# Optimization experiments

Measured on AMD Instinct MI355X. Metric: run time of the kernel, lower is better.

The kernel has to match this reference:

```python
import jax, jax.numpy as jnp
import numpy as np

N_EMBD = 256


def setup_inputs() -> dict:
    key = jax.random.key(0)
    kx, kq, kk, kv = jax.random.split(key, 4)
    B, S, D = 4, 4096, N_EMBD
    scale = 1.0 / np.sqrt(D)
    x = jax.random.normal(kx, (B, S, D), dtype=jnp.float32)
    # nn.Linear(D, D, bias=False) weights; torch applies x @ W.T
    Wq = jax.random.normal(kq, (D, D), dtype=jnp.float32) * scale
    Wk = jax.random.normal(kk, (D, D), dtype=jnp.float32) * scale
    Wv = jax.random.normal(kv, (D, D), dtype=jnp.float32) * scale
    return {"x": x, "Wq": Wq, "Wk": Wk, "Wv": Wv}


def reference(x, Wq, Wk, Wv):
    B, S, D = x.shape
    q = jnp.einsum('bsd,ed->bse', x, Wq)
    k = jnp.einsum('bsd,ed->bse', x, Wk)
    v = jnp.einsum('bsd,ed->bse', x, Wv)
    scale = 1.0 / jnp.sqrt(jnp.asarray(D, dtype=x.dtype))
    scores = jnp.einsum('bqd,bkd->bqk', q, k) * scale  # [B,S,S]
    causal = jnp.tril(jnp.ones((S, S), dtype=bool))
    masked = jnp.where(causal[None, :, :], scores, jnp.asarray(-jnp.inf, dtype=scores.dtype))
    weights = jax.nn.softmax(masked, axis=-1)
    out = jnp.einsum('bqk,bkd->bqd', weights, v)
    return out
```

## Files before the change

### kernel.cpp

```cpp
#include <hip/hip_runtime.h>
#include <hip/hip_bf16.h>


#define SEQ 4096
#define DIM 256
#define NBATCH 4
#define KVBLK 64
#define KVT_BYTES 65536

#define QB_OFF   0
#define KV_OFF   (8u*1024*1024)
#define O1_OFF   (24u*1024*1024)
#define O2_OFF   (32u*1024*1024)
#define O3_OFF   (40u*1024*1024)
#define ML_OFF   (48u*1024*1024)

#define QSCALE 0.09016844f
#define DEFER_THR 11.5415603f

typedef __attribute__((ext_vector_type(8))) short bf16x8;
typedef __attribute__((ext_vector_type(4))) float f32x4;
typedef __attribute__((ext_vector_type(4))) unsigned short us4;

static __device__ inline unsigned short f2bf(float f) {
  unsigned int u = __float_as_uint(f);
  u += 0x7FFFu + ((u >> 16) & 1u);
  return (unsigned short)(u >> 16);
}
static __device__ inline float bf2f(unsigned short u) {
  return __uint_as_float(((unsigned int)u) << 16);
}

__global__ __launch_bounds__(256) void qkv_gemm(
    const float* __restrict__ x, const float* __restrict__ Wq,
    const float* __restrict__ Wk, const float* __restrict__ Wv,
    char* __restrict__ qbf, char* __restrict__ kv)
{
  __shared__ unsigned short A_lds[128][40];
  __shared__ unsigned short B_lds[3][64][40];

  const int tid = threadIdx.x;
  const int lane = tid & 63;
  const int w = tid >> 6;
  const int lo = lane & 15, hi = lane >> 4;
  const int mb = blockIdx.x * 128;
  const int nb = blockIdx.y * 64;
  const float* Ws[3] = { Wq, Wk, Wv };

  f32x4 acc[3][2][4];
#pragma unroll
  for (int z = 0; z < 3; z++)
#pragma unroll
    for (int mi = 0; mi < 2; mi++)
#pragma unroll
      for (int ni = 0; ni < 4; ni++) acc[z][mi][ni] = (f32x4){0.f, 0.f, 0.f, 0.f};

  for (int ks = 0; ks < 8; ++ks) {
    const int k0 = ks * 32;
    __syncthreads();
#pragma unroll
    for (int i = 0; i < 4; ++i) {
      int f = tid + i * 256;
      int row = f >> 3, c4 = (f & 7) * 4;
      float4 v = *(const float4*)(x + (size_t)(mb + row) * DIM + k0 + c4);
      us4 bv = { f2bf(v.x), f2bf(v.y), f2bf(v.z), f2bf(v.w) };
      *(us4*)&A_lds[row][c4] = bv;
    }
#pragma unroll
    for (int z = 0; z < 3; z++)
#pragma unroll
      for (int i = 0; i < 2; ++i) {
        int f = tid + i * 256;
        int row = f >> 3, c4 = (f & 7) * 4;
        float4 v = *(const float4*)(Ws[z] + (size_t)(nb + row) * DIM + k0 + c4);
        us4 bv = { f2bf(v.x), f2bf(v.y), f2bf(v.z), f2bf(v.w) };
        *(us4*)&B_lds[z][row][c4] = bv;
      }
    __syncthreads();
    bf16x8 a[2];
#pragma unroll
    for (int mi = 0; mi < 2; mi++) a[mi] = *(const bf16x8*)&A_lds[w * 32 + mi * 16 + lo][hi * 8];
#pragma unroll
    for (int z = 0; z < 3; z++) {
      bf16x8 bfr[4];
#pragma unroll
      for (int ni = 0; ni < 4; ni++) bfr[ni] = *(const bf16x8*)&B_lds[z][ni * 16 + lo][hi * 8];
#pragma unroll
      for (int mi = 0; mi < 2; mi++)
#pragma unroll
        for (int ni = 0; ni < 4; ni++)
          acc[z][mi][ni] = __builtin_amdgcn_mfma_f32_16x16x32_bf16(a[mi], bfr[ni], acc[z][mi][ni], 0, 0, 0);
    }
  }

#pragma unroll
  for (int mi = 0; mi < 2; mi++) {
    int r0 = mb + w * 32 + mi * 16 + hi * 4;
#pragma unroll
    for (int ni = 0; ni < 4; ni++) {
      int d = nb + ni * 16 + lo;
      int kkq = d >> 5, hiq = (d >> 3) & 3, eq = d & 7;
#pragma unroll
      for (int j = 0; j < 4; j++) {
        int srow = r0 + j;
        int s16 = srow >> 4, loq = srow & 15;
        size_t byte = ((size_t)(s16 * 8 + kkq) << 10) + ((hiq * 16 + loq) << 4) + eq * 2;
        *(unsigned short*)(qbf + byte) = f2bf(acc[0][mi][ni][j] * QSCALE);
      }
    }
  }
#pragma unroll
  for (int mi = 0; mi < 2; mi++) {
    int r0 = mb + w * 32 + mi * 16 + hi * 4;
#pragma unroll
    for (int ni = 0; ni < 4; ni++) {
      int d = nb + ni * 16 + lo;
      int kkk = d >> 5, hik = (d >> 3) & 3, ek = d & 7;
#pragma unroll
      for (int j = 0; j < 4; j++) {
        int srow = r0 + j;
        int bb = srow >> 12, sl = srow & 4095;
        int t = sl >> 6, r = sl & 63;
        int nf = r >> 4, lok = r & 15;
        size_t byte = ((size_t)(bb * 64 + t)) * KVT_BYTES +
                      ((size_t)(nf * 8 + kkk) << 10) + ((hik * 16 + lok) << 4) + ek * 2;
        *(unsigned short*)(kv + byte) = f2bf(acc[1][mi][ni][j]);
      }
    }
  }
#pragma unroll
  for (int mi = 0; mi < 2; mi++) {
    int s0 = mb + w * 32 + mi * 16 + hi * 4;
    int bb = s0 >> 12;
    int t = (s0 >> 6) & 63;
    int s_t = s0 & 63;
    int ksI = s_t >> 5;
    int hf = (s_t >> 3) & 3;
    int e0 = s_t & 7;
#pragma unroll
    for (int ni = 0; ni < 4; ni++) {
      int d = nb + ni * 16 + lo;
      int n = d >> 4;
      us4 pv = { f2bf(acc[2][mi][ni][0]), f2bf(acc[2][mi][ni][1]),
                 f2bf(acc[2][mi][ni][2]), f2bf(acc[2][mi][ni][3]) };
      size_t byte = ((size_t)(bb * 64 + t)) * KVT_BYTES + 32768 +
                    ((size_t)(ksI * 16 + n) << 10) + ((hf * 16 + lo) << 4) + e0 * 2;
      *(us4*)(kv + byte) = pv;
    }
  }
}

__global__ __launch_bounds__(512, 1) void attn_fa(
    const char* __restrict__ qbf, const char* __restrict__ kv,
    float* __restrict__ out, unsigned short* __restrict__ o1,
    unsigned short* __restrict__ o2, unsigned short* __restrict__ o3,
    float* __restrict__ ml)
{
  __shared__ char KV_lds[2][KVT_BYTES];
  __shared__ unsigned short P_lds[8][16][72];

  const int tid = threadIdx.x;
  const int lane = tid & 63;
  const int w = tid >> 6;
  const int lo = lane & 15, hi = lane >> 4;
  const int id = blockIdx.x;
  const int x = id & 7;
  const int b = x >> 1;
  const int v = id >> 3;
  const int p = v & 15;
  const int cbase = ((v >> 4) << 1) | (x & 1);

  const char* kv_base = kv + (size_t)b * 64 * KVT_BYTES;

  auto stageKV = [&](int t, int buf) {
    const char* src = kv_base + (size_t)t * KVT_BYTES + tid * 16;
    char* dst = &KV_lds[buf][0] + tid * 16;
#pragma unroll
    for (int i = 0; i < 8; ++i) {
      __builtin_amdgcn_global_load_lds(
          (const __attribute__((address_space(1))) void*)(src + i * 8192),
          (__attribute__((address_space(3))) void*)(dst + i * 8192),
          16, 0, 0);
    }
  };

  for (int task = 0; task < 2; ++task) {
    const int u = task ? (15 - p) + 16 : p;
    const int cc = task ? (3 - cbase) : cbase;
    const int nt = 2 * u + 2;
    const int t0 = (nt * cc) >> 2;
    const int t1 = (nt * (cc + 1)) >> 2;
    const int qrow0 = u * 128 + w * 16;
    const int rbase = b * SEQ + qrow0;
    float* mlc = ml + (size_t)cc * 16384 * 2;

    if (t0 >= t1) {
      if (lane < 16) {
        mlc[(size_t)(rbase + lane) * 2 + 0] = -3e38f;
        mlc[(size_t)(rbase + lane) * 2 + 1] = 0.f;
      }
      if (cc == 0) {
#pragma unroll
        for (int j = 0; j < 16; j++)
#pragma unroll
          for (int n = 0; n < 4; n++)
            out[(size_t)(rbase + j) * DIM + n * 64 + lane] = 0.f;
      }
      continue;
    }

    bf16x8 qf[8];
    {
      const char* qp = qbf + ((size_t)(b * 256 + u * 8 + w) << 13) + lane * 16;
#pragma unroll
      for (int kk = 0; kk < 8; kk++)
        qf[kk] = *(const bf16x8*)(qp + kk * 1024);
    }

    stageKV(t0, 0);
    if (t0 + 1 < t1) stageKV(t0 + 1, 1);

    float m_run[4], l_run[4];
#pragma unroll
    for (int j = 0; j < 4; j++) { m_run[j] = -3e38f; l_run[j] = 0.f; }
    f32x4 o_acc[16];
#pragma unroll
    for (int n = 0; n < 16; n++) o_acc[n] = (f32x4){0.f, 0.f, 0.f, 0.f};

    for (int t = t0; t < t1; ++t) {
      const int cur = (t - t0) & 1;

      if (t + 1 < t1) {
        asm volatile("s_waitcnt vmcnt(8)" ::: "memory");
      } else {
        asm volatile("s_waitcnt vmcnt(0)" ::: "memory");
      }
      __builtin_amdgcn_sched_barrier(0);
      __builtin_amdgcn_s_barrier();

      const char* kt = &KV_lds[cur][0] + lane * 16;

      f32x4 sf[4];
      __builtin_amdgcn_s_setprio(1);
#pragma unroll
      for (int nf = 0; nf < 4; nf++) {
        bf16x8 kf[8];
#pragma unroll
        for (int kk = 0; kk < 8; kk++)
          kf[kk] = *(const bf16x8*)(kt + ((nf * 8 + kk) << 10));
        f32x4 a = (f32x4){0.f, 0.f, 0.f, 0.f};
#pragma unroll
        for (int kk = 0; kk < 8; kk++)
          a = __builtin_amdgcn_mfma_f32_16x16x32_bf16(qf[kk], kf[kk], a, 0, 0, 0);
        sf[nf] = a;
      }
      __builtin_amdgcn_s_setprio(0);

      const char* vt = &KV_lds[cur][32768] + lane * 16;
      bf16x8 va[16];
#pragma unroll
      for (int i = 0; i < 16; i++)
        va[i] = *(const bf16x8*)(vt + (i << 10));

      if ((t * KVBLK + KVBLK - 1) > qrow0) {
#pragma unroll
        for (int nf = 0; nf < 4; nf++) {
          int kg = t * KVBLK + nf * 16 + lo;
#pragma unroll
          for (int j = 0; j < 4; j++) {
            int qg = qrow0 + hi * 4 + j;
            if (kg > qg) sf[nf][j] = -__builtin_inff();
          }
        }
      }

      float vnew[4];
#pragma unroll
      for (int j = 0; j < 4; j++) {
        float m = fmaxf(fmaxf(sf[0][j], sf[1][j]), fmaxf(sf[2][j], sf[3][j]));
        m = fmaxf(m, __shfl_xor(m, 1));
        m = fmaxf(m, __shfl_xor(m, 2));
        m = fmaxf(m, __shfl_xor(m, 4));
        m = fmaxf(m, __shfl_xor(m, 8));
        vnew[j] = m;
      }
      bool grow = false;
#pragma unroll
      for (int j = 0; j < 4; j++) grow = grow || (vnew[j] > m_run[j] + DEFER_THR);
      if (__any(grow)) {
#pragma unroll
        for (int j = 0; j < 4; j++) {
          float mn = fmaxf(m_run[j], vnew[j]);
          float alpha = exp2f(m_run[j] - mn);
          m_run[j] = mn;
          l_run[j] *= alpha;
#pragma unroll
          for (int n = 0; n < 16; n++) o_acc[n][j] *= alpha;
        }
      }
#pragma unroll
      for (int j = 0; j < 4; j++) {
        float sum = 0.f;
#pragma unroll
        for (int nf = 0; nf < 4; nf++) {
          sf[nf][j] = exp2f(sf[nf][j] - m_run[j]);
          sum += sf[nf][j];
        }
        l_run[j] += sum;
      }

#pragma unroll
      for (int nf = 0; nf < 4; nf++)
#pragma unroll
        for (int j = 0; j < 4; j++)
          P_lds[w][hi * 4 + j][nf * 16 + lo] = f2bf(sf[nf][j]);
      asm volatile("s_waitcnt lgkmcnt(0)" ::: "memory");
      __builtin_amdgcn_sched_barrier(0);
      bf16x8 pa0 = *(const bf16x8*)&P_lds[w][lo][hi * 8];
      bf16x8 pa1 = *(const bf16x8*)&P_lds[w][lo][32 + hi * 8];
      asm volatile("s_waitcnt lgkmcnt(0)" ::: "memory");
      __builtin_amdgcn_sched_barrier(0);

      __builtin_amdgcn_s_setprio(1);
#pragma unroll
      for (int g = 0; g < 4; g++) {
        bf16x8 vb[4];
#pragma unroll
        for (int k = 0; k < 4; k++)
          vb[k] = *(const bf16x8*)(vt + ((16 + g * 4 + k) << 10));
#pragma unroll
        for (int k = 0; k < 4; k++) {
          int n = g * 4 + k;
          o_acc[n] = __builtin_amdgcn_mfma_f32_16x16x32_bf16(pa0, va[n], o_acc[n], 0, 0, 0);
          o_acc[n] = __builtin_amdgcn_mfma_f32_16x16x32_bf16(pa1, vb[k], o_acc[n], 0, 0, 0);
        }
      }
      __builtin_amdgcn_s_setprio(0);

      __builtin_amdgcn_sched_barrier(0);
      __builtin_amdgcn_s_barrier();
      if (t + 2 < t1) stageKV(t + 2, cur);
    }

    unsigned short* opc = (cc == 1) ? o1 : (cc == 2) ? o2 : o3;
#pragma unroll
    for (int j = 0; j < 4; j++) {
      float lsum = l_run[j];
      lsum += __shfl_xor(lsum, 1);
      lsum += __shfl_xor(lsum, 2);
      lsum += __shfl_xor(lsum, 4);
      lsum += __shfl_xor(lsum, 8);
      int r = rbase + hi * 4 + j;
      float inv = (lsum > 0.f) ? 1.f / lsum : 0.f;
      if (cc == 0) {
        float* orow = out + (size_t)r * DIM;
#pragma unroll
        for (int n = 0; n < 16; n++)
          orow[n * 16 + lo] = o_acc[n][j] * inv;
      } else {
        unsigned short* orow = opc + (size_t)r * DIM;
#pragma unroll
        for (int n = 0; n < 16; n++)
          orow[n * 16 + lo] = f2bf(o_acc[n][j] * inv);
      }
      if (lo == 0) {
        mlc[(size_t)r * 2 + 0] = m_run[j];
        mlc[(size_t)r * 2 + 1] = lsum;
      }
    }
  }
}

__global__ __launch_bounds__(256) void merge4(
    const float* __restrict__ ml,
    const unsigned short* __restrict__ o1, const unsigned short* __restrict__ o2,
    const unsigned short* __restrict__ o3, float* __restrict__ out)
{
  int r = blockIdx.x * 4 + (threadIdx.x >> 6);
  int c4 = (threadIdx.x & 63) * 4;
  float m0 = ml[(size_t)r*2],           l0 = ml[(size_t)r*2+1];
  float m1 = ml[(size_t)(16384+r)*2],   l1 = ml[(size_t)(16384+r)*2+1];
  float m2 = ml[(size_t)(32768+r)*2],   l2 = ml[(size_t)(32768+r)*2+1];
  float m3 = ml[(size_t)(49152+r)*2],   l3 = ml[(size_t)(49152+r)*2+1];
  float M = fmaxf(fmaxf(m0, m1), fmaxf(m2, m3));
  float w0 = l0 * exp2f(m0 - M);
  float w1 = l1 * exp2f(m1 - M);
  float w2 = l2 * exp2f(m2 - M);
  float w3 = l3 * exp2f(m3 - M);
  float inv = 1.f / (w0 + w1 + w2 + w3);
  float4 o0 = *(const float4*)(out + (size_t)r * DIM + c4);
  us4 a  = *(const us4*)(o1 + (size_t)r * DIM + c4);
  us4 bq = *(const us4*)(o2 + (size_t)r * DIM + c4);
  us4 cq = *(const us4*)(o3 + (size_t)r * DIM + c4);
  float4 res;
  res.x = (w0*o0.x + w1*bf2f(a.x) + w2*bf2f(bq.x) + w3*bf2f(cq.x)) * inv;
  res.y = (w0*o0.y + w1*bf2f(a.y) + w2*bf2f(bq.y) + w3*bf2f(cq.y)) * inv;
  res.z = (w0*o0.z + w1*bf2f(a.z) + w2*bf2f(bq.z) + w3*bf2f(cq.z)) * inv;
  res.w = (w0*o0.w + w1*bf2f(a.w) + w2*bf2f(bq.w) + w3*bf2f(cq.w)) * inv;
  *(float4*)(out + (size_t)r * DIM + c4) = res;
}

extern "C" void kernel_launch(void* const* d_in, const int* in_sizes, int n_in,
                              void* d_out, int out_size, void* d_ws, size_t ws_size,
                              hipStream_t stream) {
  const float* x  = (const float*)d_in[0];
  const float* Wq = (const float*)d_in[1];
  const float* Wk = (const float*)d_in[2];
  const float* Wv = (const float*)d_in[3];
  char* ws = (char*)d_ws;
  char* qbf = ws + QB_OFF;
  char* kv  = ws + KV_OFF;
  unsigned short* o1 = (unsigned short*)(ws + O1_OFF);
  unsigned short* o2 = (unsigned short*)(ws + O2_OFF);
  unsigned short* o3 = (unsigned short*)(ws + O3_OFF);
  float* ml = (float*)(ws + ML_OFF);
  float* out = (float*)d_out;

  qkv_gemm<<<dim3(128, 4), 256, 0, stream>>>(x, Wq, Wk, Wv, qbf, kv);
  attn_fa<<<dim3(256), 512, 0, stream>>>(qbf, kv, out, o1, o2, o3, ml);
  merge4<<<dim3(4096), 256, 0, stream>>>(ml, o1, o2, o3, out);
}
```

Measured before the change: 96.08 us.

## Compute transposed QK^T scores so each lane owns one query row

Swaps the MFMA operands so the score tile is K·Q^T, giving each lane a single query row with 16 key values. The per-row max and sum reductions then take two cross-lane shuffles instead of four per row, and the running max and sum become scalars per lane. P is packed into LDS with v_cvt_pk_bf16_f32 as 32-bit writes instead of 16 scalar bf16 stores. In exchange, rescaling the output accumulator and the final normalization now need per-row shuffles to fetch alpha and inv.

Measured after the change: 87.21 us. -9.2%, faster.

```diff
diff --git a/kernel.cpp b/kernel.cpp
--- a/kernel.cpp
+++ b/kernel.cpp
@@ -220,9 +220,7 @@
     stageKV(t0, 0);
     if (t0 + 1 < t1) stageKV(t0 + 1, 1);
 
-    float m_run[4], l_run[4];
-#pragma unroll
-    for (int j = 0; j < 4; j++) { m_run[j] = -3e38f; l_run[j] = 0.f; }
+    float m_run = -3e38f, l_run = 0.f;
     f32x4 o_acc[16];
 #pragma unroll
     for (int n = 0; n < 16; n++) o_acc[n] = (f32x4){0.f, 0.f, 0.f, 0.f};
@@ -240,7 +238,7 @@
 
       const char* kt = &KV_lds[cur][0] + lane * 16;
 
-      f32x4 sf[4];
+      f32x4 sfT[4];
       __builtin_amdgcn_s_setprio(1);
 #pragma unroll
       for (int nf = 0; nf < 4; nf++) {
@@ -251,8 +249,8 @@
         f32x4 a = (f32x4){0.f, 0.f, 0.f, 0.f};
 #pragma unroll
         for (int kk = 0; kk < 8; kk++)
-          a = __builtin_amdgcn_mfma_f32_16x16x32_bf16(qf[kk], kf[kk], a, 0, 0, 0);
-        sf[nf] = a;
+          a = __builtin_amdgcn_mfma_f32_16x16x32_bf16(kf[kk], qf[kk], a, 0, 0, 0);
+        sfT[nf] = a;
       }
       __builtin_amdgcn_s_setprio(0);
 
@@ -263,57 +261,59 @@
         va[i] = *(const bf16x8*)(vt + (i << 10));
 
       if ((t * KVBLK + KVBLK - 1) > qrow0) {
+        int qg = qrow0 + lo;
 #pragma unroll
         for (int nf = 0; nf < 4; nf++) {
-          int kg = t * KVBLK + nf * 16 + lo;
 #pragma unroll
           for (int j = 0; j < 4; j++) {
-            int qg = qrow0 + hi * 4 + j;
-            if (kg > qg) sf[nf][j] = -__builtin_inff();
+            int kg = t * KVBLK + nf * 16 + hi * 4 + j;
+            if (kg > qg) sfT[nf][j] = -__builtin_inff();
           }
         }
       }
 
-      float vnew[4];
-#pragma unroll
-      for (int j = 0; j < 4; j++) {
-        float m = fmaxf(fmaxf(sf[0][j], sf[1][j]), fmaxf(sf[2][j], sf[3][j]));
-        m = fmaxf(m, __shfl_xor(m, 1));
-        m = fmaxf(m, __shfl_xor(m, 2));
-        m = fmaxf(m, __shfl_xor(m, 4));
-        m = fmaxf(m, __shfl_xor(m, 8));
-        vnew[j] = m;
-      }
-      bool grow = false;
-#pragma unroll
-      for (int j = 0; j < 4; j++) grow = grow || (vnew[j] > m_run[j] + DEFER_THR);
-      if (__any(grow)) {
+      float vnew = sfT[0][0];
+#pragma unroll
+      for (int nf = 0; nf < 4; nf++)
+#pragma unroll
+        for (int j = 0; j < 4; j++) vnew = fmaxf(vnew, sfT[nf][j]);
+      vnew = fmaxf(vnew, __shfl_xor(vnew, 16));
+      vnew = fmaxf(vnew, __shfl_xor(vnew, 32));
+
+      if (__any(vnew > m_run + DEFER_THR)) {
+        float mn = fmaxf(m_run, vnew);
+        float alpha = exp2f(m_run - mn);
+        m_run = mn;
+        l_run *= alpha;
 #pragma unroll
         for (int j = 0; j < 4; j++) {
-          float mn = fmaxf(m_run[j], vnew[j]);
-          float alpha = exp2f(m_run[j] - mn);
-          m_run[j] = mn;
-          l_run[j] *= alpha;
-#pragma unroll
-          for (int n = 0; n < 16; n++) o_acc[n][j] *= alpha;
+          float aj = __shfl(alpha, (lane & 48) + ((lane >> 4) & 3) * 4 + j);
+#pragma unroll
+          for (int n = 0; n < 16; n++) o_acc[n][j] *= aj;
         }
       }
-#pragma unroll
-      for (int j = 0; j < 4; j++) {
+      {
         float sum = 0.f;
 #pragma unroll
-        for (int nf = 0; nf < 4; nf++) {
-          sf[nf][j] = exp2f(sf[nf][j] - m_run[j]);
-          sum += sf[nf][j];
+        for (int nf = 0; nf < 4; nf++)
+#pragma unroll
+          for (int j = 0; j < 4; j++) {
+            sfT[nf][j] = exp2f(sfT[nf][j] - m_run);
+            sum += sfT[nf][j];
+          }
+        l_run += sum;
+      }
+
+#pragma unroll
+      for (int nf = 0; nf < 4; nf++) {
+#pragma unroll
+        for (int h2 = 0; h2 < 2; h2++) {
+          unsigned int pk;
+          asm("v_cvt_pk_bf16_f32 %0, %1, %2"
+              : "=v"(pk) : "v"(sfT[nf][h2 * 2]), "v"(sfT[nf][h2 * 2 + 1]));
+          *(unsigned int*)&P_lds[w][lo][nf * 16 + hi * 4 + h2 * 2] = pk;
         }
-        l_run[j] += sum;
-      }
-
-#pragma unroll
-      for (int nf = 0; nf < 4; nf++)
-#pragma unroll
-        for (int j = 0; j < 4; j++)
-          P_lds[w][hi * 4 + j][nf * 16 + lo] = f2bf(sf[nf][j]);
+      }
       asm volatile("s_waitcnt lgkmcnt(0)" ::: "memory");
       __builtin_amdgcn_sched_barrier(0);
       bf16x8 pa0 = *(const bf16x8*)&P_lds[w][lo][hi * 8];
@@ -342,31 +342,30 @@
       if (t + 2 < t1) stageKV(t + 2, cur);
     }
 
+    l_run += __shfl_xor(l_run, 16);
+    l_run += __shfl_xor(l_run, 32);
+    float inv = (l_run > 0.f) ? 1.f / l_run : 0.f;
+
     unsigned short* opc = (cc == 1) ? o1 : (cc == 2) ? o2 : o3;
 #pragma unroll
     for (int j = 0; j < 4; j++) {
-      float lsum = l_run[j];
-      lsum += __shfl_xor(lsum, 1);
-      lsum += __shfl_xor(lsum, 2);
-      lsum += __shfl_xor(lsum, 4);
-      lsum += __shfl_xor(lsum, 8);
+      float invj = __shfl(inv, (lane & 48) + ((lane >> 4) & 3) * 4 + j);
       int r = rbase + hi * 4 + j;
-      float inv = (lsum > 0.f) ? 1.f / lsum : 0.f;
       if (cc == 0) {
         float* orow = out + (size_t)r * DIM;
 #pragma unroll
         for (int n = 0; n < 16; n++)
-          orow[n * 16 + lo] = o_acc[n][j] * inv;
+          orow[n * 16 + lo] = o_acc[n][j] * invj;
       } else {
         unsigned short* orow = opc + (size_t)r * DIM;
 #pragma unroll
         for (int n = 0; n < 16; n++)
-          orow[n * 16 + lo] = f2bf(o_acc[n][j] * inv);
-      }
-      if (lo == 0) {
-        mlc[(size_t)r * 2 + 0] = m_run[j];
-        mlc[(size_t)r * 2 + 1] = lsum;
-      }
+          orow[n * 16 + lo] = f2bf(o_acc[n][j] * invj);
+      }
+    }
+    if (hi == 0) {
+      mlc[(size_t)(rbase + lo) * 2 + 0] = m_run;
+      mlc[(size_t)(rbase + lo) * 2 + 1] = l_run;
     }
   }
 }
```
